# Optimization experiments

Measured on AMD Instinct MI355X. Metric: run time of the kernel, lower is better.

Reference implementation:

```python
import jax, jax.numpy as jnp
import numpy as np

C = 512      # filters
G = 32       # groups
EPS = 1e-6

def setup_inputs() -> dict:
    key = jax.random.key(0)
    ks = jax.random.split(key, 10)
    B, H, W = 2, 64, 64
    inputs = jax.random.normal(ks[0], (B, H, W, C), dtype=jnp.float32)
    scale = 1.0 / np.sqrt(C)
    def w(k):
        return jax.random.normal(k, (C, C), dtype=jnp.float32) * scale
    return {
        "inputs": inputs,
        "gn_gamma": jnp.ones((C,), jnp.float32),
        "gn_beta": jnp.zeros((C,), jnp.float32),
        "wq": w(ks[1]), "bq": jnp.zeros((C,), jnp.float32),
        "wk": w(ks[2]), "bk": jnp.zeros((C,), jnp.float32),
        "wv": w(ks[3]), "bv": jnp.zeros((C,), jnp.float32),
        "wo": w(ks[4]), "bo": jnp.zeros((C,), jnp.float32),
    }

def _group_norm(x, gamma, beta):
    B, H, W, c = x.shape
    xg = x.reshape(B, H, W, G, c // G)
    mean = jnp.mean(xg, axis=(1, 2, 4), keepdims=True)
    var = jnp.var(xg, axis=(1, 2, 4), keepdims=True)
    xg = (xg - mean) * jax.lax.rsqrt(var + EPS)
    return xg.reshape(B, H, W, c) * gamma + beta

def reference(inputs, gn_gamma, gn_beta, wq, bq, wk, bk, wv, bv, wo, bo):
    B, H, W, c = inputs.shape
    x = _group_norm(inputs, gn_gamma, gn_beta)
    # 1x1 convs == per-pixel linear layers
    q = (x @ wq + bq).reshape(B, H * W, c)
    k = (x @ wk + bk).reshape(B, H * W, c)
    v = (x @ wv + bv).reshape(B, H * W, c)
    q = q * jnp.asarray(1.0 / np.sqrt(float(c)), q.dtype)
    scores = jnp.einsum('bnc,bmc->bnm', q, k).astype(jnp.float32)  # [B,N,N]
    probs = jax.nn.softmax(scores, axis=-1).astype(inputs.dtype)
    attn = jnp.einsum('bnm,bmc->bnc', probs, v)
    out = attn.reshape(B, H, W, c) @ wo + bo
    return out + inputs
```

## Files before the change

kernel.cpp:

```cpp
#include <hip/hip_runtime.h>
#include <math.h>

typedef __bf16 bf16;
typedef __bf16 bf16x8 __attribute__((ext_vector_type(8)));
typedef float  f32x4  __attribute__((ext_vector_type(4)));

#define DEV __device__ __forceinline__
#define VMCNT(n) asm volatile("s_waitcnt vmcnt(" #n ")" ::: "memory")
#define CFENCE  asm volatile("" ::: "memory")
#define BAR()   { CFENCE; __builtin_amdgcn_s_barrier(); CFENCE; }

DEV void gload_lds16(const bf16* g, bf16* l) {
  __builtin_amdgcn_global_load_lds(
      (const __attribute__((address_space(1))) void*)g,
      (__attribute__((address_space(3))) void*)l, 16, 0, 0);
}

#define OFF_STATS 0UL
#define OFF_WOT   1024UL
#define OFF_BIASQ 525312UL
#define OFF_WTQKV 531456UL
#define OFF_XN    2104320UL
#define OFF_QKV   10492928UL
#define OFF_VT    35658752UL
#define OFF_S     44047360UL
#define OFF_P0    2104320UL
#define OFF_P1    18881536UL
#define OFF_ATTN  44047360UL
#define OFF_GNP   44047360UL

__global__ __launch_bounds__(256) void gn_part_k(const float* __restrict__ x,
                                                 float2* __restrict__ part) {
  const int blk = blockIdx.x;
  const int chunk = blk & 15;
  const int bg = blk >> 4;
  const int b = bg >> 5, g = bg & 31;
  const int t = threadIdx.x;
  const int p = chunk * 256 + t;
  const float* xp = x + (size_t)b * (4096 * 512) + (size_t)p * 512 + g * 16;
  float4 v0 = *(const float4*)(xp);
  float4 v1 = *(const float4*)(xp + 4);
  float4 v2 = *(const float4*)(xp + 8);
  float4 v3 = *(const float4*)(xp + 12);
  float s  = v0.x + v0.y + v0.z + v0.w + v1.x + v1.y + v1.z + v1.w
           + v2.x + v2.y + v2.z + v2.w + v3.x + v3.y + v3.z + v3.w;
  float ss = v0.x*v0.x + v0.y*v0.y + v0.z*v0.z + v0.w*v0.w
           + v1.x*v1.x + v1.y*v1.y + v1.z*v1.z + v1.w*v1.w
           + v2.x*v2.x + v2.y*v2.y + v2.z*v2.z + v2.w*v2.w
           + v3.x*v3.x + v3.y*v3.y + v3.z*v3.z + v3.w*v3.w;
#pragma unroll
  for (int off = 32; off; off >>= 1) {
    s  += __shfl_xor(s, off);
    ss += __shfl_xor(ss, off);
  }
  __shared__ float rs[4], rss[4];
  const int w = t >> 6, l = t & 63;
  if (l == 0) { rs[w] = s; rss[w] = ss; }
  __syncthreads();
  if (t == 0)
    part[blk] = make_float2(rs[0] + rs[1] + rs[2] + rs[3],
                            rss[0] + rss[1] + rss[2] + rss[3]);
}

__global__ void gn_finish_k(const float2* __restrict__ part,
                            float2* __restrict__ stats) {
  const int g = threadIdx.x;
  float s = 0.f, ss = 0.f;
#pragma unroll
  for (int c = 0; c < 16; ++c) {
    float2 p = part[g * 16 + c];
    s += p.x; ss += p.y;
  }
  float mean = s * (1.0f / 65536.0f);
  float var  = ss * (1.0f / 65536.0f) - mean * mean;
  stats[g] = make_float2(mean, 1.0f / sqrtf(var + 1e-6f));
}

__global__ __launch_bounds__(256) void gn_apply_k(const float* __restrict__ x,
                                                  const float2* __restrict__ stats,
                                                  const float* __restrict__ gamma,
                                                  const float* __restrict__ beta,
                                                  bf16* __restrict__ xn) {
  size_t i = ((size_t)blockIdx.x * 256 + threadIdx.x) * 8;
  const int c = (int)(i & 511);
  const int b = (int)(i >> 21);
  float2 st = stats[b * 32 + (c >> 4)];
  float4 xa = *(const float4*)(x + i);
  float4 xb = *(const float4*)(x + i + 4);
  float4 ga = *(const float4*)(gamma + c);
  float4 gb = *(const float4*)(gamma + c + 4);
  float4 ba = *(const float4*)(beta + c);
  float4 bb = *(const float4*)(beta + c + 4);
  bf16x8 o;
  o[0] = (bf16)((xa.x - st.x) * st.y * ga.x + ba.x);
  o[1] = (bf16)((xa.y - st.x) * st.y * ga.y + ba.y);
  o[2] = (bf16)((xa.z - st.x) * st.y * ga.z + ba.z);
  o[3] = (bf16)((xa.w - st.x) * st.y * ga.w + ba.w);
  o[4] = (bf16)((xb.x - st.x) * st.y * gb.x + bb.x);
  o[5] = (bf16)((xb.y - st.x) * st.y * gb.y + bb.y);
  o[6] = (bf16)((xb.z - st.x) * st.y * gb.z + bb.z);
  o[7] = (bf16)((xb.w - st.x) * st.y * gb.w + bb.w);
  *(bf16x8*)(xn + i) = o;
}

__global__ void prep_w_k(const float* __restrict__ wq, const float* __restrict__ wk,
                         const float* __restrict__ wv, const float* __restrict__ wo,
                         bf16* __restrict__ wt_qkv, bf16* __restrict__ wot, float qscale) {
  const int z = blockIdx.z;
  const float* W = (z == 0) ? wq : (z == 1) ? wk : (z == 2) ? wv : wo;
  bf16* dst = (z < 3) ? (wt_qkv + (size_t)z * 512 * 512) : wot;
  const float s = (z == 0) ? qscale : 1.0f;
  __shared__ float tile[32][33];
  const int i0 = blockIdx.y * 32;
  const int o0 = blockIdx.x * 32;
#pragma unroll
  for (int r = threadIdx.y; r < 32; r += 8)
    tile[r][threadIdx.x] = W[(size_t)(i0 + r) * 512 + o0 + threadIdx.x];
  __syncthreads();
#pragma unroll
  for (int r = threadIdx.y; r < 32; r += 8)
    dst[(size_t)(o0 + r) * 512 + i0 + threadIdx.x] = (bf16)(tile[threadIdx.x][r] * s);
}

__global__ void prep_bias_k(const float* __restrict__ bq, const float* __restrict__ bk,
                            const float* __restrict__ bv, float* __restrict__ bias_qkv,
                            float qscale) {
  int i = blockIdx.x * 256 + threadIdx.x;
  float v = (i < 512) ? bq[i] * qscale : (i < 1024) ? bk[i - 512] : bv[i - 1024];
  bias_qkv[i] = v;
}

__global__ void transpose_v_k(const bf16* __restrict__ qkv, bf16* __restrict__ vt) {
  __shared__ bf16 tile[32][33];
  const int z = blockIdx.z;
  const int n0 = blockIdx.x * 32, d0 = blockIdx.y * 32;
  const bf16* src = qkv + (size_t)z * 4096 * 1536 + 1024;
#pragma unroll
  for (int r = threadIdx.y; r < 32; r += 8)
    tile[r][threadIdx.x] = src[(size_t)(n0 + r) * 1536 + d0 + threadIdx.x];
  __syncthreads();
  bf16* dst = vt + (size_t)z * 512 * 4096;
#pragma unroll
  for (int r = threadIdx.y; r < 32; r += 8)
    dst[(size_t)(d0 + r) * 4096 + n0 + threadIdx.x] = tile[threadIdx.x][r];
}

__global__ __launch_bounds__(256) void softmax_k(bf16* __restrict__ S) {
  const int t = threadIdx.x;
  bf16* p = S + (size_t)blockIdx.x * 4096 + t * 16;
  bf16x8 u0 = *(const bf16x8*)p;
  bf16x8 u1 = *(const bf16x8*)(p + 8);
  float v[16];
#pragma unroll
  for (int j = 0; j < 8; ++j) { v[j] = (float)u0[j]; v[j + 8] = (float)u1[j]; }
  float m = v[0];
#pragma unroll
  for (int j = 1; j < 16; ++j) m = fmaxf(m, v[j]);
#pragma unroll
  for (int off = 32; off; off >>= 1) m = fmaxf(m, __shfl_xor(m, off));
  __shared__ float red[4];
  const int w = t >> 6, l = t & 63;
  if (l == 0) red[w] = m;
  __syncthreads();
  m = fmaxf(fmaxf(red[0], red[1]), fmaxf(red[2], red[3]));
  __syncthreads();
  float s = 0.f;
#pragma unroll
  for (int j = 0; j < 16; ++j) { v[j] = __expf(v[j] - m); s += v[j]; }
#pragma unroll
  for (int off = 32; off; off >>= 1) s += __shfl_xor(s, off);
  if (l == 0) red[w] = s;
  __syncthreads();
  s = red[0] + red[1] + red[2] + red[3];
  const float inv = 1.0f / s;
#pragma unroll
  for (int j = 0; j < 8; ++j) { u0[j] = (bf16)(v[j] * inv); u1[j] = (bf16)(v[j + 8] * inv); }
  *(bf16x8*)p = u0;
  *(bf16x8*)(p + 8) = u1;
}

__global__ __launch_bounds__(256) void reduce_pv_k(const float* __restrict__ p0,
                                                   const float* __restrict__ p1,
                                                   bf16* __restrict__ attn) {
  size_t i = ((size_t)blockIdx.x * 256 + threadIdx.x) * 8;
  float4 a = *(const float4*)(p0 + i);
  float4 b = *(const float4*)(p0 + i + 4);
  float4 c = *(const float4*)(p1 + i);
  float4 d = *(const float4*)(p1 + i + 4);
  bf16x8 o;
  o[0] = (bf16)(a.x + c.x); o[1] = (bf16)(a.y + c.y);
  o[2] = (bf16)(a.z + c.z); o[3] = (bf16)(a.w + c.w);
  o[4] = (bf16)(b.x + d.x); o[5] = (bf16)(b.y + d.y);
  o[6] = (bf16)(b.z + d.z); o[7] = (bf16)(b.w + d.w);
  *(bf16x8*)(attn + i) = o;
}

template <int BM, int BN, int EPI, int GX, int GY, int GZ>
__global__ __launch_bounds__(256, 2) void gemm_nt(
    const bf16* __restrict__ A, int lda, long sAz,
    const bf16* __restrict__ B, int ldb, long sBz,
    void* __restrict__ C, int ldc, long sCz,
    int nk,
    const float* __restrict__ bias,
    const float* __restrict__ resid) {
  constexpr int WM = BM / 2, WN = BN / 2;
  constexpr int FM = BM / 32, FN = BN / 32;
  constexpr int NWG = GX * GY * GZ;
  constexpr int CPX = NWG / 8;
  __shared__ alignas(16) bf16 As[2][BM * 64];
  __shared__ alignas(16) bf16 Bs[2][BN * 64];

  const int lin = blockIdx.x;
  const int wid = (lin & 7) * CPX + (lin >> 3);
  const int bx = wid % GX;
  const int by = (wid / GX) % GY;
  const int bz = wid / (GX * GY);

  const int t = threadIdx.x;
  const bf16* Aq = A + (size_t)bz * sAz + (size_t)by * BM * lda;
  const bf16* Bq = B + (size_t)bz * sBz + (size_t)bx * BN * ldb;

  const int srow = t >> 3;
  const int sg   = (t & 7) ^ (srow & 7);

  auto stage = [&](int buf, int kt) {
    const int k0 = kt * 64 + sg * 8;
#pragma unroll
    for (int i = 0; i < BM / 32; ++i)
      gload_lds16(Aq + (size_t)(i * 32 + srow) * lda + k0, &As[buf][i * 2048 + t * 8]);
#pragma unroll
    for (int i = 0; i < BN / 32; ++i)
      gload_lds16(Bq + (size_t)(i * 32 + srow) * ldb + k0, &Bs[buf][i * 2048 + t * 8]);
  };

  const int l = t & 63, w = t >> 6;
  const int wr = w >> 1, wc = w & 1;
  const int lr = l & 15, kh = l >> 4;
  const int rs = lr & 7;

  f32x4 acc[FM][FN] = {};

  stage(0, 0);
  for (int kt = 0; kt < nk; ++kt) {
    __syncthreads();
    if (kt + 1 < nk) stage((kt + 1) & 1, kt + 1);
    const int buf = kt & 1;
    bf16x8 a[2][FM], b[2][FN];
#pragma unroll
    for (int h = 0; h < 2; ++h) {
      const int g = ((h * 4 + kh) ^ rs) * 8;
#pragma unroll
      for (int m = 0; m < FM; ++m)
        a[h][m] = *(const bf16x8*)(&As[buf][(wr * WM + m * 16 + lr) * 64 + g]);
#pragma unroll
      for (int n = 0; n < FN; ++n)
        b[h][n] = *(const bf16x8*)(&Bs[buf][(wc * WN + n * 16 + lr) * 64 + g]);
    }
#pragma unroll
    for (int h = 0; h < 2; ++h)
#pragma unroll
      for (int m = 0; m < FM; ++m)
#pragma unroll
        for (int n = 0; n < FN; ++n)
          acc[m][n] = __builtin_amdgcn_mfma_f32_16x16x32_bf16(a[h][m], b[h][n], acc[m][n], 0, 0, 0);
  }

  const int gr0 = by * BM + wr * WM + kh * 4;
  const int gc0 = bx * BN + wc * WN + lr;
#pragma unroll
  for (int m = 0; m < FM; ++m)
#pragma unroll
    for (int n = 0; n < FN; ++n) {
      const int c = gc0 + n * 16;
      float bv = 0.f;
      if constexpr (EPI >= 1) bv = bias[c];
#pragma unroll
      for (int j = 0; j < 4; ++j) {
        const int r = gr0 + m * 16 + j;
        float val = acc[m][n][j] + bv;
        if constexpr (EPI == 2) {
          float* Cf = (float*)C + (size_t)bz * sCz;
          Cf[(size_t)r * ldc + c] = val + resid[(size_t)r * ldc + c];
        } else {
          bf16* Cb = (bf16*)C + (size_t)bz * sCz;
          Cb[(size_t)r * ldc + c] = (bf16)val;
        }
      }
    }
}

template <int BM, int BN, int WR, int WC, int EPI, int GX, int GY, int GZ, int KS>
__global__ __launch_bounds__(512, 2) void gemm_8p(
    const bf16* __restrict__ A, int lda, long sAz,
    const bf16* __restrict__ B, int ldb, long sBz,
    void* __restrict__ C0, void* __restrict__ C1, int ldc, long sCz,
    int nt) {
  constexpr int WM = BM / WR, WN = BN / WC;
  constexpr int FM = WM / 16, FN = WN / 16;
  constexpr int HM = FM / 2, HN = FN / 2;
  constexpr int LA = BM / 128, LB = BN / 128;
  constexpr int NWG = GX * KS * GY * GZ;
  constexpr int CPX = NWG / 8;
  static_assert(WR * WC == 8, "8 waves");
  static_assert(LA == 2 && (LB == 1 || LB == 2), "vmcnt literals");

  __shared__ alignas(16) bf16 As[2][BM * 64];
  __shared__ alignas(16) bf16 Bs[2][BN * 64];

  const int t = threadIdx.x;
  const int lin = blockIdx.x;
  const int wid = (lin & 7) * CPX + (lin >> 3);
  const int bx = wid % GX;
  const int ks = (wid / GX) % KS;
  const int by = (wid / (GX * KS)) % GY;
  const int bz = wid / (GX * KS * GY);

  const long kOff = (long)ks * nt * 64;
  const bf16* Aq = A + (size_t)bz * sAz + (size_t)by * BM * lda + kOff;
  const bf16* Bq = B + (size_t)bz * sBz + (size_t)bx * BN * ldb + kOff;

  const int srow = t >> 3;
  const int sgr  = (t & 7) ^ (srow & 7);

  auto stageA = [&](int buf, int tile, int half) {
    const bf16* src = Aq + (size_t)(half * (BM / 2) + srow) * lda + tile * 64 + sgr * 8;
    bf16* dst = &As[buf][(half * (BM / 2)) * 64] + t * 8;
#pragma unroll
    for (int j = 0; j < LA; ++j)
      gload_lds16(src + (size_t)(j * 64) * lda, dst + j * 4096);
  };
  auto stageB = [&](int buf, int tile, int half) {
    const bf16* src = Bq + (size_t)(half * (BN / 2) + srow) * ldb + tile * 64 + sgr * 8;
    bf16* dst = &Bs[buf][(half * (BN / 2)) * 64] + t * 8;
#pragma unroll
    for (int j = 0; j < LB; ++j)
      gload_lds16(src + (size_t)(j * 64) * ldb, dst + j * 4096);
  };

  const int l = t & 63, w = t >> 6;
  const int wr = w / WC, wc = w % WC;
  const int lr = l & 15, kh = l >> 4;
  const int rs8 = lr & 7;

  bf16x8 af[HM][2], bf_[HN][2];
  auto readA = [&](int buf, int qm) {
#pragma unroll
    for (int i = 0; i < HM; ++i)
#pragma unroll
      for (int h = 0; h < 2; ++h)
        af[i][h] = *(const bf16x8*)(
            &As[buf][(wr * WM + qm * (WM / 2) + i * 16 + lr) * 64 + (((h * 4 + kh) ^ rs8) * 8)]);
  };
  auto readB = [&](int buf, int qn) {
#pragma unroll
    for (int j = 0; j < HN; ++j)
#pragma unroll
      for (int h = 0; h < 2; ++h)
        bf_[j][h] = *(const bf16x8*)(
            &Bs[buf][(wc * WN + qn * (WN / 2) + j * 16 + lr) * 64 + (((h * 4 + kh) ^ rs8) * 8)]);
  };

  f32x4 acc[FM][FN] = {};

#define MFMAQ(QM, QN) { \
  __builtin_amdgcn_s_setprio(1); \
  _Pragma("unroll") for (int ii = 0; ii < HM; ++ii) \
  _Pragma("unroll") for (int jj = 0; jj < HN; ++jj) \
  _Pragma("unroll") for (int h = 0; h < 2; ++h) \
    acc[(QM)*HM + ii][(QN)*HN + jj] = __builtin_amdgcn_mfma_f32_16x16x32_bf16( \
        af[ii][h], bf_[jj][h], acc[(QM)*HM + ii][(QN)*HN + jj], 0, 0, 0); \
  __builtin_amdgcn_s_setprio(0); }
#define WAIT_LB() { if constexpr (LB == 1) VMCNT(1); else VMCNT(2); }

  stageA(0, 0, 0); stageA(0, 0, 1); stageB(0, 0, 0); stageB(0, 0, 1);
  WAIT_LB();
  BAR();

  const int half = nt >> 1;
  for (int i = 0; i < half; ++i) {
    const int t1 = 2 * i + 1, t2 = 2 * i + 2;
    const bool last = (i == half - 1);
    readA(0, 0); readB(0, 0);
    stageA(1, t1, 0);
    BAR();
    MFMAQ(0, 0);
    BAR();
    readA(0, 1);
    stageA(1, t1, 1);
    BAR();
    MFMAQ(1, 0);
    VMCNT(4);
    BAR();
    readB(0, 1);
    stageB(1, t1, 0);
    BAR();
    MFMAQ(1, 1);
    BAR();
    readA(0, 0);
    stageB(1, t1, 1);
    BAR();
    MFMAQ(0, 1);
    WAIT_LB();
    BAR();
    readA(1, 0); readB(1, 0);
    if (!last) stageA(0, t2, 0);
    BAR();
    MFMAQ(0, 0);
    BAR();
    readA(1, 1);
    if (!last) stageA(0, t2, 1);
    BAR();
    MFMAQ(1, 0);
    if (last) { VMCNT(0); } else { VMCNT(4); }
    BAR();
    readB(1, 1);
    if (!last) stageB(0, t2, 0);
    BAR();
    MFMAQ(1, 1);
    BAR();
    readA(1, 0);
    if (!last) stageB(0, t2, 1);
    BAR();
    MFMAQ(0, 1);
    WAIT_LB();
    BAR();
  }
#undef MFMAQ
#undef WAIT_LB

  const int gr0 = by * BM + wr * WM + kh * 4;
  const int gc0 = bx * BN + wc * WN + lr;
#pragma unroll
  for (int m = 0; m < FM; ++m)
#pragma unroll
    for (int n = 0; n < FN; ++n) {
      const int c = gc0 + n * 16;
#pragma unroll
      for (int j = 0; j < 4; ++j) {
        const int r = gr0 + m * 16 + j;
        if constexpr (EPI == 0) {
          bf16* Cb = (bf16*)C0 + (size_t)bz * sCz;
          Cb[(size_t)r * ldc + c] = (bf16)acc[m][n][j];
        } else {
          float* Cf = (float*)(ks ? C1 : C0) + (size_t)bz * sCz;
          Cf[(size_t)r * ldc + c] = acc[m][n][j];
        }
      }
    }
}

extern "C" void kernel_launch(void* const* d_in, const int* in_sizes, int n_in,
                              void* d_out, int out_size, void* d_ws, size_t ws_size,
                              hipStream_t stream) {
  const float* x     = (const float*)d_in[0];
  const float* gamma = (const float*)d_in[1];
  const float* beta  = (const float*)d_in[2];
  const float* wq = (const float*)d_in[3];
  const float* bq = (const float*)d_in[4];
  const float* wk = (const float*)d_in[5];
  const float* bk = (const float*)d_in[6];
  const float* wv = (const float*)d_in[7];
  const float* bv = (const float*)d_in[8];
  const float* wo = (const float*)d_in[9];
  const float* bo = (const float*)d_in[10];
  float* out = (float*)d_out;
  char* ws = (char*)d_ws;

  float2* stats    = (float2*)(ws + OFF_STATS);
  bf16*   wot      = (bf16*)(ws + OFF_WOT);
  float*  bias_qkv = (float*)(ws + OFF_BIASQ);
  bf16*   wt_qkv   = (bf16*)(ws + OFF_WTQKV);
  bf16*   xn       = (bf16*)(ws + OFF_XN);
  bf16*   qkv      = (bf16*)(ws + OFF_QKV);
  bf16*   vt       = (bf16*)(ws + OFF_VT);
  bf16*   S        = (bf16*)(ws + OFF_S);
  float*  p0       = (float*)(ws + OFF_P0);
  float*  p1       = (float*)(ws + OFF_P1);
  bf16*   attn     = (bf16*)(ws + OFF_ATTN);
  float2* gn_part  = (float2*)(ws + OFF_GNP);

  const float qscale = 0.04419417382415922f;

  prep_w_k<<<dim3(16, 16, 4), dim3(32, 8), 0, stream>>>(wq, wk, wv, wo, wt_qkv, wot, qscale);
  prep_bias_k<<<6, 256, 0, stream>>>(bq, bk, bv, bias_qkv, qscale);
  gn_part_k<<<1024, 256, 0, stream>>>(x, gn_part);
  gn_finish_k<<<1, 64, 0, stream>>>(gn_part, stats);
  gn_apply_k<<<2048, 256, 0, stream>>>(x, stats, gamma, beta, xn);

  gemm_nt<128, 128, 1, 12, 64, 1><<<768, 256, 0, stream>>>(
      xn, 512, 0, wt_qkv, 512, 0, qkv, 1536, 0, 512 / 64, bias_qkv, nullptr);

  gemm_8p<256, 256, 2, 4, 0, 16, 16, 2, 1><<<512, 512, 0, stream>>>(
      qkv, 1536, 4096L * 1536, qkv + 512, 1536, 4096L * 1536,
      S, nullptr, 4096, 4096L * 4096, 512 / 64);

  softmax_k<<<8192, 256, 0, stream>>>(S);

  transpose_v_k<<<dim3(128, 16, 2), dim3(32, 8), 0, stream>>>(qkv, vt);

  gemm_8p<256, 128, 4, 2, 3, 4, 16, 2, 2><<<256, 512, 0, stream>>>(
      S, 4096, 4096L * 4096, vt, 4096, 512L * 4096,
      p0, p1, 512, 4096L * 512, 2048 / 64);

  reduce_pv_k<<<2048, 256, 0, stream>>>(p0, p1, attn);

  gemm_nt<64, 128, 2, 4, 128, 1><<<512, 256, 0, stream>>>(
      attn, 512, 0, wot, 512, 0, out, 512, 0, 512 / 64, bo, x);
}
```

Before: 176.5 us.

## Fuse exponentiation into QK^T epilogue and defer softmax normalization to PV reduce

Result: faster. 163.1 us (-7.6%).

```diff
diff --git a/kernel.cpp b/kernel.cpp
--- a/kernel.cpp
+++ b/kernel.cpp
@@ -24,6 +24,8 @@
 #define OFF_QKV   10492928UL
 #define OFF_VT    35658752UL
 #define OFF_S     44047360UL
+#define OFF_LSUM  111156224UL
+#define OFF_INVL  113253376UL
 #define OFF_P0    2104320UL
 #define OFF_P1    18881536UL
 #define OFF_ATTN  44047360UL
@@ -145,53 +147,34 @@
     dst[(size_t)(d0 + r) * 4096 + n0 + threadIdx.x] = tile[threadIdx.x][r];
 }
 
-__global__ __launch_bounds__(256) void softmax_k(bf16* __restrict__ S) {
-  const int t = threadIdx.x;
-  bf16* p = S + (size_t)blockIdx.x * 4096 + t * 16;
-  bf16x8 u0 = *(const bf16x8*)p;
-  bf16x8 u1 = *(const bf16x8*)(p + 8);
-  float v[16];
-#pragma unroll
-  for (int j = 0; j < 8; ++j) { v[j] = (float)u0[j]; v[j + 8] = (float)u1[j]; }
-  float m = v[0];
-#pragma unroll
-  for (int j = 1; j < 16; ++j) m = fmaxf(m, v[j]);
-#pragma unroll
-  for (int off = 32; off; off >>= 1) m = fmaxf(m, __shfl_xor(m, off));
-  __shared__ float red[4];
-  const int w = t >> 6, l = t & 63;
-  if (l == 0) red[w] = m;
-  __syncthreads();
-  m = fmaxf(fmaxf(red[0], red[1]), fmaxf(red[2], red[3]));
-  __syncthreads();
+__global__ __launch_bounds__(256) void inv_l_k(const float* __restrict__ lsum,
+                                               float* __restrict__ invl) {
+  const int r = blockIdx.x * 256 + threadIdx.x;
+  const float* p = lsum + (size_t)r * 64;
   float s = 0.f;
 #pragma unroll
-  for (int j = 0; j < 16; ++j) { v[j] = __expf(v[j] - m); s += v[j]; }
-#pragma unroll
-  for (int off = 32; off; off >>= 1) s += __shfl_xor(s, off);
-  if (l == 0) red[w] = s;
-  __syncthreads();
-  s = red[0] + red[1] + red[2] + red[3];
-  const float inv = 1.0f / s;
-#pragma unroll
-  for (int j = 0; j < 8; ++j) { u0[j] = (bf16)(v[j] * inv); u1[j] = (bf16)(v[j + 8] * inv); }
-  *(bf16x8*)p = u0;
-  *(bf16x8*)(p + 8) = u1;
+  for (int k = 0; k < 64; k += 4) {
+    float4 v = *(const float4*)(p + k);
+    s += v.x + v.y + v.z + v.w;
+  }
+  invl[r] = 1.0f / s;
 }
 
 __global__ __launch_bounds__(256) void reduce_pv_k(const float* __restrict__ p0,
                                                    const float* __restrict__ p1,
+                                                   const float* __restrict__ invl,
                                                    bf16* __restrict__ attn) {
   size_t i = ((size_t)blockIdx.x * 256 + threadIdx.x) * 8;
+  const float il = invl[i >> 9];
   float4 a = *(const float4*)(p0 + i);
   float4 b = *(const float4*)(p0 + i + 4);
   float4 c = *(const float4*)(p1 + i);
   float4 d = *(const float4*)(p1 + i + 4);
   bf16x8 o;
-  o[0] = (bf16)(a.x + c.x); o[1] = (bf16)(a.y + c.y);
-  o[2] = (bf16)(a.z + c.z); o[3] = (bf16)(a.w + c.w);
-  o[4] = (bf16)(b.x + d.x); o[5] = (bf16)(b.y + d.y);
-  o[6] = (bf16)(b.z + d.z); o[7] = (bf16)(b.w + d.w);
+  o[0] = (bf16)((a.x + c.x) * il); o[1] = (bf16)((a.y + c.y) * il);
+  o[2] = (bf16)((a.z + c.z) * il); o[3] = (bf16)((a.w + c.w) * il);
+  o[4] = (bf16)((b.x + d.x) * il); o[5] = (bf16)((b.y + d.y) * il);
+  o[6] = (bf16)((b.z + d.z) * il); o[7] = (bf16)((b.w + d.w) * il);
   *(bf16x8*)(attn + i) = o;
 }
 
@@ -294,7 +277,7 @@
     const bf16* __restrict__ A, int lda, long sAz,
     const bf16* __restrict__ B, int ldb, long sBz,
     void* __restrict__ C0, void* __restrict__ C1, int ldc, long sCz,
-    int nt) {
+    int nt, float* __restrict__ LS) {
   constexpr int WM = BM / WR, WN = BN / WC;
   constexpr int FM = WM / 16, FN = WN / 16;
   constexpr int HM = FM / 2, HN = FN / 2;
@@ -430,23 +413,63 @@
 
   const int gr0 = by * BM + wr * WM + kh * 4;
   const int gc0 = bx * BN + wc * WN + lr;
-#pragma unroll
-  for (int m = 0; m < FM; ++m)
-#pragma unroll
-    for (int n = 0; n < FN; ++n) {
-      const int c = gc0 + n * 16;
-#pragma unroll
-      for (int j = 0; j < 4; ++j) {
-        const int r = gr0 + m * 16 + j;
-        if constexpr (EPI == 0) {
-          bf16* Cb = (bf16*)C0 + (size_t)bz * sCz;
-          Cb[(size_t)r * ldc + c] = (bf16)acc[m][n][j];
-        } else {
-          float* Cf = (float*)(ks ? C1 : C0) + (size_t)bz * sCz;
-          Cf[(size_t)r * ldc + c] = acc[m][n][j];
+  if constexpr (EPI == 4) {
+    bf16* Cb = (bf16*)C0 + (size_t)bz * sCz;
+    float rsum[FM][4];
+#pragma unroll
+    for (int m = 0; m < FM; ++m)
+#pragma unroll
+      for (int j = 0; j < 4; ++j) rsum[m][j] = 0.f;
+#pragma unroll
+    for (int m = 0; m < FM; ++m)
+#pragma unroll
+      for (int n = 0; n < FN; ++n) {
+        const int c = gc0 + n * 16;
+#pragma unroll
+        for (int j = 0; j < 4; ++j) {
+          const int r = gr0 + m * 16 + j;
+          float e = __expf(acc[m][n][j]);
+          Cb[(size_t)r * ldc + c] = (bf16)e;
+          rsum[m][j] += e;
         }
       }
+#pragma unroll
+    for (int m = 0; m < FM; ++m)
+#pragma unroll
+      for (int j = 0; j < 4; ++j) {
+        float v = rsum[m][j];
+        v += __shfl_xor(v, 1); v += __shfl_xor(v, 2);
+        v += __shfl_xor(v, 4); v += __shfl_xor(v, 8);
+        rsum[m][j] = v;
+      }
+    if (lr == 0) {
+#pragma unroll
+      for (int m = 0; m < FM; ++m)
+#pragma unroll
+        for (int j = 0; j < 4; ++j) {
+          const int r = gr0 + m * 16 + j;
+          LS[((size_t)bz * 4096 + r) * (GX * WC) + bx * WC + wc] = rsum[m][j];
+        }
     }
+  } else {
+#pragma unroll
+    for (int m = 0; m < FM; ++m)
+#pragma unroll
+      for (int n = 0; n < FN; ++n) {
+        const int c = gc0 + n * 16;
+#pragma unroll
+        for (int j = 0; j < 4; ++j) {
+          const int r = gr0 + m * 16 + j;
+          if constexpr (EPI == 0) {
+            bf16* Cb = (bf16*)C0 + (size_t)bz * sCz;
+            Cb[(size_t)r * ldc + c] = (bf16)acc[m][n][j];
+          } else {
+            float* Cf = (float*)(ks ? C1 : C0) + (size_t)bz * sCz;
+            Cf[(size_t)r * ldc + c] = acc[m][n][j];
+          }
+        }
+      }
+  }
 }
 
 extern "C" void kernel_launch(void* const* d_in, const int* in_sizes, int n_in,
@@ -474,6 +497,8 @@
   bf16*   qkv      = (bf16*)(ws + OFF_QKV);
   bf16*   vt       = (bf16*)(ws + OFF_VT);
   bf16*   S        = (bf16*)(ws + OFF_S);
+  float*  lsum     = (float*)(ws + OFF_LSUM);
+  float*  invl     = (float*)(ws + OFF_INVL);
   float*  p0       = (float*)(ws + OFF_P0);
   float*  p1       = (float*)(ws + OFF_P1);
   bf16*   attn     = (bf16*)(ws + OFF_ATTN);
@@ -490,19 +515,19 @@
   gemm_nt<128, 128, 1, 12, 64, 1><<<768, 256, 0, stream>>>(
       xn, 512, 0, wt_qkv, 512, 0, qkv, 1536, 0, 512 / 64, bias_qkv, nullptr);
 
-  gemm_8p<256, 256, 2, 4, 0, 16, 16, 2, 1><<<512, 512, 0, stream>>>(
+  gemm_8p<256, 256, 2, 4, 4, 16, 16, 2, 1><<<512, 512, 0, stream>>>(
       qkv, 1536, 4096L * 1536, qkv + 512, 1536, 4096L * 1536,
-      S, nullptr, 4096, 4096L * 4096, 512 / 64);
-
-  softmax_k<<<8192, 256, 0, stream>>>(S);
+      S, nullptr, 4096, 4096L * 4096, 512 / 64, lsum);
+
+  inv_l_k<<<32, 256, 0, stream>>>(lsum, invl);
 
   transpose_v_k<<<dim3(128, 16, 2), dim3(32, 8), 0, stream>>>(qkv, vt);
 
   gemm_8p<256, 128, 4, 2, 3, 4, 16, 2, 2><<<256, 512, 0, stream>>>(
       S, 4096, 4096L * 4096, vt, 4096, 512L * 4096,
-      p0, p1, 512, 4096L * 512, 2048 / 64);
-
-  reduce_pv_k<<<2048, 256, 0, stream>>>(p0, p1, attn);
+      p0, p1, 512, 4096L * 512, 2048 / 64, nullptr);
+
+  reduce_pv_k<<<2048, 256, 0, stream>>>(p0, p1, invl, attn);
 
   gemm_nt<64, 128, 2, 4, 128, 1><<<512, 256, 0, stream>>>(
       attn, 512, 0, wot, 512, 0, out, 512, 0, 512 / 64, bo, x);
```

## Fuse exp into QK GEMM, defer softmax normalization into PV epilogue

Applied to the files above, without the earlier changes.

Result: faster. 169.1 us (-4.2%).

```diff
diff --git a/kernel.cpp b/kernel.cpp
--- a/kernel.cpp
+++ b/kernel.cpp
@@ -24,9 +24,8 @@
 #define OFF_QKV   10492928UL
 #define OFF_VT    35658752UL
 #define OFF_S     44047360UL
-#define OFF_P0    2104320UL
-#define OFF_P1    18881536UL
-#define OFF_ATTN  44047360UL
+#define OFF_INVL  111156224UL
+#define OFF_ATTN  2104320UL
 #define OFF_GNP   44047360UL
 
 __global__ __launch_bounds__(256) void gn_part_k(const float* __restrict__ x,
@@ -145,54 +144,23 @@
     dst[(size_t)(d0 + r) * 4096 + n0 + threadIdx.x] = tile[threadIdx.x][r];
 }
 
-__global__ __launch_bounds__(256) void softmax_k(bf16* __restrict__ S) {
-  const int t = threadIdx.x;
-  bf16* p = S + (size_t)blockIdx.x * 4096 + t * 16;
+__global__ __launch_bounds__(256) void rowsum_k(const bf16* __restrict__ S,
+                                                float* __restrict__ invl) {
+  const int r = blockIdx.x;
+  const bf16* p = S + (size_t)r * 4096 + threadIdx.x * 16;
   bf16x8 u0 = *(const bf16x8*)p;
   bf16x8 u1 = *(const bf16x8*)(p + 8);
-  float v[16];
-#pragma unroll
-  for (int j = 0; j < 8; ++j) { v[j] = (float)u0[j]; v[j + 8] = (float)u1[j]; }
-  float m = v[0];
-#pragma unroll
-  for (int j = 1; j < 16; ++j) m = fmaxf(m, v[j]);
-#pragma unroll
-  for (int off = 32; off; off >>= 1) m = fmaxf(m, __shfl_xor(m, off));
+  float s = 0.f;
+#pragma unroll
+  for (int j = 0; j < 8; ++j) s += (float)u0[j] + (float)u1[j];
+#pragma unroll
+  for (int off = 32; off; off >>= 1) s += __shfl_xor(s, off);
   __shared__ float red[4];
-  const int w = t >> 6, l = t & 63;
-  if (l == 0) red[w] = m;
-  __syncthreads();
-  m = fmaxf(fmaxf(red[0], red[1]), fmaxf(red[2], red[3]));
-  __syncthreads();
-  float s = 0.f;
-#pragma unroll
-  for (int j = 0; j < 16; ++j) { v[j] = __expf(v[j] - m); s += v[j]; }
-#pragma unroll
-  for (int off = 32; off; off >>= 1) s += __shfl_xor(s, off);
+  const int w = threadIdx.x >> 6, l = threadIdx.x & 63;
   if (l == 0) red[w] = s;
   __syncthreads();
-  s = red[0] + red[1] + red[2] + red[3];
-  const float inv = 1.0f / s;
-#pragma unroll
-  for (int j = 0; j < 8; ++j) { u0[j] = (bf16)(v[j] * inv); u1[j] = (bf16)(v[j + 8] * inv); }
-  *(bf16x8*)p = u0;
-  *(bf16x8*)(p + 8) = u1;
-}
-
-__global__ __launch_bounds__(256) void reduce_pv_k(const float* __restrict__ p0,
-                                                   const float* __restrict__ p1,
-                                                   bf16* __restrict__ attn) {
-  size_t i = ((size_t)blockIdx.x * 256 + threadIdx.x) * 8;
-  float4 a = *(const float4*)(p0 + i);
-  float4 b = *(const float4*)(p0 + i + 4);
-  float4 c = *(const float4*)(p1 + i);
-  float4 d = *(const float4*)(p1 + i + 4);
-  bf16x8 o;
-  o[0] = (bf16)(a.x + c.x); o[1] = (bf16)(a.y + c.y);
-  o[2] = (bf16)(a.z + c.z); o[3] = (bf16)(a.w + c.w);
-  o[4] = (bf16)(b.x + d.x); o[5] = (bf16)(b.y + d.y);
-  o[6] = (bf16)(b.z + d.z); o[7] = (bf16)(b.w + d.w);
-  *(bf16x8*)(attn + i) = o;
+  if (threadIdx.x == 0)
+    invl[r] = 1.0f / (red[0] + red[1] + red[2] + red[3]);
 }
 
 template <int BM, int BN, int EPI, int GX, int GY, int GZ>
@@ -273,7 +241,7 @@
     for (int n = 0; n < FN; ++n) {
       const int c = gc0 + n * 16;
       float bv = 0.f;
-      if constexpr (EPI >= 1) bv = bias[c];
+      if constexpr (EPI == 1 || EPI == 2) bv = bias[c];
 #pragma unroll
       for (int j = 0; j < 4; ++j) {
         const int r = gr0 + m * 16 + j;
@@ -281,6 +249,9 @@
         if constexpr (EPI == 2) {
           float* Cf = (float*)C + (size_t)bz * sCz;
           Cf[(size_t)r * ldc + c] = val + resid[(size_t)r * ldc + c];
+        } else if constexpr (EPI == 5) {
+          bf16* Cb = (bf16*)C + (size_t)bz * sCz;
+          Cb[(size_t)r * ldc + c] = (bf16)(acc[m][n][j] * bias[bz * 4096 + r]);
         } else {
           bf16* Cb = (bf16*)C + (size_t)bz * sCz;
           Cb[(size_t)r * ldc + c] = (bf16)val;
@@ -289,17 +260,17 @@
     }
 }
 
-template <int BM, int BN, int WR, int WC, int EPI, int GX, int GY, int GZ, int KS>
+template <int BM, int BN, int WR, int WC, int EPI, int GX, int GY, int GZ>
 __global__ __launch_bounds__(512, 2) void gemm_8p(
     const bf16* __restrict__ A, int lda, long sAz,
     const bf16* __restrict__ B, int ldb, long sBz,
-    void* __restrict__ C0, void* __restrict__ C1, int ldc, long sCz,
+    void* __restrict__ C0, int ldc, long sCz,
     int nt) {
   constexpr int WM = BM / WR, WN = BN / WC;
   constexpr int FM = WM / 16, FN = WN / 16;
   constexpr int HM = FM / 2, HN = FN / 2;
   constexpr int LA = BM / 128, LB = BN / 128;
-  constexpr int NWG = GX * KS * GY * GZ;
+  constexpr int NWG = GX * GY * GZ;
   constexpr int CPX = NWG / 8;
   static_assert(WR * WC == 8, "8 waves");
   static_assert(LA == 2 && (LB == 1 || LB == 2), "vmcnt literals");
@@ -311,13 +282,11 @@
   const int lin = blockIdx.x;
   const int wid = (lin & 7) * CPX + (lin >> 3);
   const int bx = wid % GX;
-  const int ks = (wid / GX) % KS;
-  const int by = (wid / (GX * KS)) % GY;
-  const int bz = wid / (GX * KS * GY);
-
-  const long kOff = (long)ks * nt * 64;
-  const bf16* Aq = A + (size_t)bz * sAz + (size_t)by * BM * lda + kOff;
-  const bf16* Bq = B + (size_t)bz * sBz + (size_t)bx * BN * ldb + kOff;
+  const int by = (wid / GX) % GY;
+  const int bz = wid / (GX * GY);
+
+  const bf16* Aq = A + (size_t)bz * sAz + (size_t)by * BM * lda;
+  const bf16* Bq = B + (size_t)bz * sBz + (size_t)bx * BN * ldb;
 
   const int srow = t >> 3;
   const int sgr  = (t & 7) ^ (srow & 7);
@@ -430,6 +399,7 @@
 
   const int gr0 = by * BM + wr * WM + kh * 4;
   const int gc0 = bx * BN + wc * WN + lr;
+  bf16* Cb = (bf16*)C0 + (size_t)bz * sCz;
 #pragma unroll
   for (int m = 0; m < FM; ++m)
 #pragma unroll
@@ -438,12 +408,10 @@
 #pragma unroll
       for (int j = 0; j < 4; ++j) {
         const int r = gr0 + m * 16 + j;
-        if constexpr (EPI == 0) {
-          bf16* Cb = (bf16*)C0 + (size_t)bz * sCz;
+        if constexpr (EPI == 6) {
+          Cb[(size_t)r * ldc + c] = (bf16)__expf(acc[m][n][j]);
+        } else {
           Cb[(size_t)r * ldc + c] = (bf16)acc[m][n][j];
-        } else {
-          float* Cf = (float*)(ks ? C1 : C0) + (size_t)bz * sCz;
-          Cf[(size_t)r * ldc + c] = acc[m][n][j];
         }
       }
     }
@@ -474,8 +442,7 @@
   bf16*   qkv      = (bf16*)(ws + OFF_QKV);
   bf16*   vt       = (bf16*)(ws + OFF_VT);
   bf16*   S        = (bf16*)(ws + OFF_S);
-  float*  p0       = (float*)(ws + OFF_P0);
-  float*  p1       = (float*)(ws + OFF_P1);
+  float*  invl     = (float*)(ws + OFF_INVL);
   bf16*   attn     = (bf16*)(ws + OFF_ATTN);
   float2* gn_part  = (float2*)(ws + OFF_GNP);
 
@@ -490,19 +457,17 @@
   gemm_nt<128, 128, 1, 12, 64, 1><<<768, 256, 0, stream>>>(
       xn, 512, 0, wt_qkv, 512, 0, qkv, 1536, 0, 512 / 64, bias_qkv, nullptr);
 
-  gemm_8p<256, 256, 2, 4, 0, 16, 16, 2, 1><<<512, 512, 0, stream>>>(
+  gemm_8p<256, 256, 2, 4, 6, 16, 16, 2><<<512, 512, 0, stream>>>(
       qkv, 1536, 4096L * 1536, qkv + 512, 1536, 4096L * 1536,
-      S, nullptr, 4096, 4096L * 4096, 512 / 64);
-
-  softmax_k<<<8192, 256, 0, stream>>>(S);
+      S, 4096, 4096L * 4096, 512 / 64);
+
+  rowsum_k<<<8192, 256, 0, stream>>>(S, invl);
 
   transpose_v_k<<<dim3(128, 16, 2), dim3(32, 8), 0, stream>>>(qkv, vt);
 
-  gemm_8p<256, 128, 4, 2, 3, 4, 16, 2, 2><<<256, 512, 0, stream>>>(
+  gemm_nt<128, 64, 5, 8, 32, 2><<<512, 256, 0, stream>>>(
       S, 4096, 4096L * 4096, vt, 4096, 512L * 4096,
-      p0, p1, 512, 4096L * 512, 2048 / 64);
-
-  reduce_pv_k<<<2048, 256, 0, stream>>>(p0, p1, attn);
+      attn, 512, 4096L * 512, 4096 / 64, invl, nullptr);
 
   gemm_nt<64, 128, 2, 4, 128, 1><<<512, 256, 0, stream>>>(
       attn, 512, 0, wot, 512, 0, out, 512, 0, 512 / 64, bo, x);
```

## Fuse exp into QK^T epilogue and defer softmax normalization to PV reduce

Applied to the files above, without the earlier changes.

Measured after the change: 165.1 us. -6.5%, faster.

```diff
diff --git a/kernel.cpp b/kernel.cpp
--- a/kernel.cpp
+++ b/kernel.cpp
@@ -24,6 +24,7 @@
 #define OFF_QKV   10492928UL
 #define OFF_VT    35658752UL
 #define OFF_S     44047360UL
+#define OFF_INVL  111156224UL
 #define OFF_P0    2104320UL
 #define OFF_P1    18881536UL
 #define OFF_ATTN  44047360UL
@@ -145,53 +146,40 @@
     dst[(size_t)(d0 + r) * 4096 + n0 + threadIdx.x] = tile[threadIdx.x][r];
 }
 
-__global__ __launch_bounds__(256) void softmax_k(bf16* __restrict__ S) {
-  const int t = threadIdx.x;
-  bf16* p = S + (size_t)blockIdx.x * 4096 + t * 16;
+__global__ __launch_bounds__(256) void rowsum_k(const bf16* __restrict__ S,
+                                                float* __restrict__ invl) {
+  const int r = blockIdx.x;
+  const bf16* p = S + (size_t)r * 4096 + threadIdx.x * 16;
   bf16x8 u0 = *(const bf16x8*)p;
   bf16x8 u1 = *(const bf16x8*)(p + 8);
-  float v[16];
-#pragma unroll
-  for (int j = 0; j < 8; ++j) { v[j] = (float)u0[j]; v[j + 8] = (float)u1[j]; }
-  float m = v[0];
-#pragma unroll
-  for (int j = 1; j < 16; ++j) m = fmaxf(m, v[j]);
-#pragma unroll
-  for (int off = 32; off; off >>= 1) m = fmaxf(m, __shfl_xor(m, off));
+  float s = 0.f;
+#pragma unroll
+  for (int j = 0; j < 8; ++j) s += (float)u0[j] + (float)u1[j];
+#pragma unroll
+  for (int off = 32; off; off >>= 1) s += __shfl_xor(s, off);
   __shared__ float red[4];
-  const int w = t >> 6, l = t & 63;
-  if (l == 0) red[w] = m;
-  __syncthreads();
-  m = fmaxf(fmaxf(red[0], red[1]), fmaxf(red[2], red[3]));
-  __syncthreads();
-  float s = 0.f;
-#pragma unroll
-  for (int j = 0; j < 16; ++j) { v[j] = __expf(v[j] - m); s += v[j]; }
-#pragma unroll
-  for (int off = 32; off; off >>= 1) s += __shfl_xor(s, off);
+  const int w = threadIdx.x >> 6, l = threadIdx.x & 63;
   if (l == 0) red[w] = s;
   __syncthreads();
-  s = red[0] + red[1] + red[2] + red[3];
-  const float inv = 1.0f / s;
-#pragma unroll
-  for (int j = 0; j < 8; ++j) { u0[j] = (bf16)(v[j] * inv); u1[j] = (bf16)(v[j + 8] * inv); }
-  *(bf16x8*)p = u0;
-  *(bf16x8*)(p + 8) = u1;
+  if (threadIdx.x == 0)
+    invl[r] = 1.0f / (red[0] + red[1] + red[2] + red[3]);
 }
 
 __global__ __launch_bounds__(256) void reduce_pv_k(const float* __restrict__ p0,
                                                    const float* __restrict__ p1,
+                                                   const float* __restrict__ invl,
                                                    bf16* __restrict__ attn) {
   size_t i = ((size_t)blockIdx.x * 256 + threadIdx.x) * 8;
+  const float il = invl[i >> 9];
   float4 a = *(const float4*)(p0 + i);
   float4 b = *(const float4*)(p0 + i + 4);
   float4 c = *(const float4*)(p1 + i);
   float4 d = *(const float4*)(p1 + i + 4);
   bf16x8 o;
-  o[0] = (bf16)(a.x + c.x); o[1] = (bf16)(a.y + c.y);
-  o[2] = (bf16)(a.z + c.z); o[3] = (bf16)(a.w + c.w);
-  o[4] = (bf16)(b.x + d.x); o[5] = (bf16)(b.y + d.y);
-  o[6] = (bf16)(b.z + d.z); o[7] = (bf16)(b.w + d.w);
+  o[0] = (bf16)((a.x + c.x) * il); o[1] = (bf16)((a.y + c.y) * il);
+  o[2] = (bf16)((a.z + c.z) * il); o[3] = (bf16)((a.w + c.w) * il);
+  o[4] = (bf16)((b.x + d.x) * il); o[5] = (bf16)((b.y + d.y) * il);
+  o[6] = (bf16)((b.z + d.z) * il); o[7] = (bf16)((b.w + d.w) * il);
   *(bf16x8*)(attn + i) = o;
 }
 
@@ -272,8 +260,7 @@
 #pragma unroll
     for (int n = 0; n < FN; ++n) {
       const int c = gc0 + n * 16;
-      float bv = 0.f;
-      if constexpr (EPI >= 1) bv = bias[c];
+      float bv = bias[c];
 #pragma unroll
       for (int j = 0; j < 4; ++j) {
         const int r = gr0 + m * 16 + j;
@@ -438,9 +425,9 @@
 #pragma unroll
       for (int j = 0; j < 4; ++j) {
         const int r = gr0 + m * 16 + j;
-        if constexpr (EPI == 0) {
+        if constexpr (EPI == 6) {
           bf16* Cb = (bf16*)C0 + (size_t)bz * sCz;
-          Cb[(size_t)r * ldc + c] = (bf16)acc[m][n][j];
+          Cb[(size_t)r * ldc + c] = (bf16)__expf(acc[m][n][j]);
         } else {
           float* Cf = (float*)(ks ? C1 : C0) + (size_t)bz * sCz;
           Cf[(size_t)r * ldc + c] = acc[m][n][j];
@@ -474,6 +461,7 @@
   bf16*   qkv      = (bf16*)(ws + OFF_QKV);
   bf16*   vt       = (bf16*)(ws + OFF_VT);
   bf16*   S        = (bf16*)(ws + OFF_S);
+  float*  invl     = (float*)(ws + OFF_INVL);
   float*  p0       = (float*)(ws + OFF_P0);
   float*  p1       = (float*)(ws + OFF_P1);
   bf16*   attn     = (bf16*)(ws + OFF_ATTN);
@@ -490,11 +478,11 @@
   gemm_nt<128, 128, 1, 12, 64, 1><<<768, 256, 0, stream>>>(
       xn, 512, 0, wt_qkv, 512, 0, qkv, 1536, 0, 512 / 64, bias_qkv, nullptr);
 
-  gemm_8p<256, 256, 2, 4, 0, 16, 16, 2, 1><<<512, 512, 0, stream>>>(
+  gemm_8p<256, 256, 2, 4, 6, 16, 16, 2, 1><<<512, 512, 0, stream>>>(
       qkv, 1536, 4096L * 1536, qkv + 512, 1536, 4096L * 1536,
       S, nullptr, 4096, 4096L * 4096, 512 / 64);
 
-  softmax_k<<<8192, 256, 0, stream>>>(S);
+  rowsum_k<<<8192, 256, 0, stream>>>(S, invl);
 
   transpose_v_k<<<dim3(128, 16, 2), dim3(32, 8), 0, stream>>>(qkv, vt);
 
@@ -502,7 +490,7 @@
       S, 4096, 4096L * 4096, vt, 4096, 512L * 4096,
       p0, p1, 512, 4096L * 512, 2048 / 64);
 
-  reduce_pv_k<<<2048, 256, 0, stream>>>(p0, p1, attn);
+  reduce_pv_k<<<2048, 256, 0, stream>>>(p0, p1, invl, attn);
 
   gemm_nt<64, 128, 2, 4, 128, 1><<<512, 256, 0, stream>>>(
       attn, 512, 0, wot, 512, 0, out, 512, 0, 512 / 64, bo, x);
```
